# Kernel optimization log

Measured on AMD Instinct MI355X. Metric: run time of the kernel, lower is better.

## Reference

```python
import jax, jax.numpy as jnp
import numpy as np

B, S, H, L = 64, 512, 768, 3

def setup_inputs() -> dict:
    key = jax.random.key(0)
    ks = jax.random.split(key, 6)
    hidden = jax.random.normal(ks[0], (B, S, H), dtype=jnp.float32)
    attention_mask = jnp.ones((B, S), dtype=jnp.int32)
    labels = jax.random.randint(ks[1], (B, S), 0, L)
    W = jax.random.normal(ks[2], (H, L), dtype=jnp.float32) * 0.02
    b = jnp.zeros((L,), dtype=jnp.float32)
    start_transitions = jax.random.normal(ks[3], (L,), dtype=jnp.float32) * 0.1
    end_transitions = jax.random.normal(ks[4], (L,), dtype=jnp.float32) * 0.1
    transitions = jax.random.normal(ks[5], (L, L), dtype=jnp.float32) * 0.1
    return {"hidden": hidden, "W": W, "b": b,
            "start_transitions": start_transitions,
            "end_transitions": end_transitions,
            "transitions": transitions,
            "attention_mask": attention_mask, "labels": labels}

def _crf_nll(emissions, tags, mask, start_transitions, end_transitions, transitions):
    # emissions [B,S,L], tags [B,S] int, mask [B,S] float (contiguous, mask[:,0]=1)
    em_t = jnp.transpose(emissions, (1, 0, 2))   # [S,B,L]
    tags_t = tags.T                              # [S,B]
    mask_t = mask.T                              # [S,B]

    # --- gold-path score ---
    e0 = jnp.take_along_axis(em_t[0], tags_t[0][:, None], axis=1)[:, 0]
    score0 = start_transitions[tags_t[0]] + e0   # [B]

    def gold_step(carry, inp):
        score, prev_tags, last_tags = carry
        em, tg, m = inp
        e = jnp.take_along_axis(em, tg[:, None], axis=1)[:, 0]
        t = transitions[prev_tags, tg]
        score = score + (e + t) * m
        last_tags = jnp.where(m > 0, tg, last_tags)
        return (score, tg, last_tags), None

    (score, _, last_tags), _ = jax.lax.scan(
        gold_step, (score0, tags_t[0], tags_t[0]),
        (em_t[1:], tags_t[1:], mask_t[1:]))
    score = score + end_transitions[last_tags]   # [B]

    # --- log-partition via forward algorithm ---
    alpha0 = start_transitions[None, :] + em_t[0]  # [B,L]

    def fwd_step(alpha, inp):
        em, m = inp
        # [B,prev,next]: alpha + transition + next emission
        nxt = jax.nn.logsumexp(alpha[:, :, None] + transitions[None, :, :]
                               + em[:, None, :], axis=1)
        alpha = jnp.where(m[:, None] > 0, nxt, alpha)
        return alpha, None

    alpha, _ = jax.lax.scan(fwd_step, alpha0, (em_t[1:], mask_t[1:]))
    log_z = jax.nn.logsumexp(alpha + end_transitions[None, :], axis=1)  # [B]

    return -jnp.mean(score - log_z)  # reduction='mean', negated

def reference(hidden, W, b, start_transitions, end_transitions, transitions,
              attention_mask, labels):
    # classifier (dropout is identity in eval)
    emissions = hidden @ W + b                     # [B,S,L]
    crf_labels = jnp.where(labels < 0, 0, labels)  # masked_fill(labels<0, O)
    maskf = attention_mask.astype(emissions.dtype)
    loss = _crf_nll(emissions, crf_labels, maskf,
                    start_transitions, end_transitions, transitions)
    return loss
```

## Files before the change

kernel.cpp:

```cpp
#include <hip/hip_runtime.h>
#include <math.h>

#define HD 768
#define NL 3
#define BB 64
#define SS 512
#define NEG (-1e30f)

__device__ __forceinline__ float lse3(float x, float y, float z) {
    float m = fmaxf(fmaxf(x, y), z);
    return m + __logf(__expf(x - m) + __expf(y - m) + __expf(z - m));
}

__global__ __launch_bounds__(256) void emis_kernel(
    const float* __restrict__ hidden, const float* __restrict__ W,
    const float* __restrict__ bias, float* __restrict__ em) {
    int gid  = blockIdx.x * blockDim.x + threadIdx.x;
    int wave = gid >> 6;
    int lane = threadIdx.x & 63;
    int BS = BB * SS;
    if (wave >= BS) return;
    const float4* h4 = (const float4*)(hidden + (size_t)wave * HD);
    float a0 = 0.f, a1 = 0.f, a2 = 0.f;
#pragma unroll
    for (int i = 0; i < 3; ++i) {
        int k4 = lane + 64 * i;
        float4 v = h4[k4];
        int k = k4 * 4;
        a0 = fmaf(v.x, W[(k + 0) * 3 + 0], a0);
        a1 = fmaf(v.x, W[(k + 0) * 3 + 1], a1);
        a2 = fmaf(v.x, W[(k + 0) * 3 + 2], a2);
        a0 = fmaf(v.y, W[(k + 1) * 3 + 0], a0);
        a1 = fmaf(v.y, W[(k + 1) * 3 + 1], a1);
        a2 = fmaf(v.y, W[(k + 1) * 3 + 2], a2);
        a0 = fmaf(v.z, W[(k + 2) * 3 + 0], a0);
        a1 = fmaf(v.z, W[(k + 2) * 3 + 1], a1);
        a2 = fmaf(v.z, W[(k + 2) * 3 + 2], a2);
        a0 = fmaf(v.w, W[(k + 3) * 3 + 0], a0);
        a1 = fmaf(v.w, W[(k + 3) * 3 + 1], a1);
        a2 = fmaf(v.w, W[(k + 3) * 3 + 2], a2);
    }
#pragma unroll
    for (int off = 32; off; off >>= 1) {
        a0 += __shfl_down(a0, off);
        a1 += __shfl_down(a1, off);
        a2 += __shfl_down(a2, off);
    }
    if (lane == 0) {
        int b = wave >> 9;
        int s = wave & (SS - 1);
        float* o = em + ((size_t)b * SS + s) * NL;
        o[0] = a0 + bias[0];
        o[1] = a1 + bias[1];
        o[2] = a2 + bias[2];
    }
}

__global__ __launch_bounds__(64) void crf_scan_kernel(
    const float* __restrict__ em,
    const int* __restrict__ mask,
    const int* __restrict__ labels,
    const float* __restrict__ startT, const float* __restrict__ endT,
    const float* __restrict__ trans, float* __restrict__ part) {
    int b = blockIdx.x;
    int l = threadIdx.x;

    float T00 = trans[0], T01 = trans[1], T02 = trans[2];
    float T10 = trans[3], T11 = trans[4], T12 = trans[5];
    float T20 = trans[6], T21 = trans[7], T22 = trans[8];

    const float* emb = em + (size_t)b * SS * NL;
    const int*   tg  = labels + b * SS;
    const int*   mk  = mask + b * SS;
    int s0 = l * 8;

    const float4* ep = (const float4*)(emb + (size_t)s0 * NL);
    float4 E0 = ep[0], E1 = ep[1], E2 = ep[2];
    float4 E3 = ep[3], E4 = ep[4], E5 = ep[5];
    int4 ta  = ((const int4*)(tg + s0))[0];
    int4 tb4 = ((const int4*)(tg + s0))[1];
    int4 ma  = ((const int4*)(mk + s0))[0];
    int4 mb4 = ((const int4*)(mk + s0))[1];
    int pv = (l > 0) ? tg[s0 - 1] : 0;
    int prev = pv < 0 ? 0 : pv;

    float P00, P01, P02, P10, P11, P12, P20, P21, P22;
    float gold = 0.f;
    int last_s = -1, last_t = 0;

#define GOLD(kk, ee0, ee1, ee2, tt, mm, ACT)                                   \
    int t = (tt) < 0 ? 0 : (tt);                                               \
    bool act = (ACT) && ((mm) != 0);                                           \
    {                                                                          \
        float ev = (t == 0) ? (ee0) : ((t == 1) ? (ee1) : (ee2));              \
        float r0 = (t == 0) ? T00 : ((t == 1) ? T01 : T02);                    \
        float r1 = (t == 0) ? T10 : ((t == 1) ? T11 : T12);                    \
        float r2 = (t == 0) ? T20 : ((t == 1) ? T21 : T22);                    \
        float tpt = (prev == 0) ? r0 : ((prev == 1) ? r1 : r2);                \
        gold += act ? (ev + tpt) : 0.f;                                        \
        last_t = act ? t : last_t;                                             \
        last_s = act ? (s0 + (kk)) : last_s;                                   \
        prev = t;                                                              \
    }

#define STEP0(ee0, ee1, ee2, tt, mm) {                                         \
    GOLD(0, ee0, ee1, ee2, tt, mm, (s0 > 0))                                   \
    P00 = act ? (T00 + (ee0)) : 0.f;                                           \
    P01 = act ? (T01 + (ee1)) : NEG;                                           \
    P02 = act ? (T02 + (ee2)) : NEG;                                           \
    P10 = act ? (T10 + (ee0)) : NEG;                                           \
    P11 = act ? (T11 + (ee1)) : 0.f;                                           \
    P12 = act ? (T12 + (ee2)) : NEG;                                           \
    P20 = act ? (T20 + (ee0)) : NEG;                                           \
    P21 = act ? (T21 + (ee1)) : NEG;                                           \
    P22 = act ? (T22 + (ee2)) : 0.f;                                           \
}

#define STEPK(kk, ee0, ee1, ee2, tt, mm) {                                     \
    GOLD(kk, ee0, ee1, ee2, tt, mm, true)                                      \
    float n00 = lse3(P00 + T00, P01 + T10, P02 + T20) + (ee0);                 \
    float n01 = lse3(P00 + T01, P01 + T11, P02 + T21) + (ee1);                 \
    float n02 = lse3(P00 + T02, P01 + T12, P02 + T22) + (ee2);                 \
    float n10 = lse3(P10 + T00, P11 + T10, P12 + T20) + (ee0);                 \
    float n11 = lse3(P10 + T01, P11 + T11, P12 + T21) + (ee1);                 \
    float n12 = lse3(P10 + T02, P11 + T12, P12 + T22) + (ee2);                 \
    float n20 = lse3(P20 + T00, P21 + T10, P22 + T20) + (ee0);                 \
    float n21 = lse3(P20 + T01, P21 + T11, P22 + T21) + (ee1);                 \
    float n22 = lse3(P20 + T02, P21 + T12, P22 + T22) + (ee2);                 \
    P00 = act ? n00 : P00; P01 = act ? n01 : P01; P02 = act ? n02 : P02;       \
    P10 = act ? n10 : P10; P11 = act ? n11 : P11; P12 = act ? n12 : P12;       \
    P20 = act ? n20 : P20; P21 = act ? n21 : P21; P22 = act ? n22 : P22;       \
}

    STEP0(    E0.x, E0.y, E0.z, ta.x,  ma.x)
    STEPK(1,  E0.w, E1.x, E1.y, ta.y,  ma.y)
    STEPK(2,  E1.z, E1.w, E2.x, ta.z,  ma.z)
    STEPK(3,  E2.y, E2.z, E2.w, ta.w,  ma.w)
    STEPK(4,  E3.x, E3.y, E3.z, tb4.x, mb4.x)
    STEPK(5,  E3.w, E4.x, E4.y, tb4.y, mb4.y)
    STEPK(6,  E4.z, E4.w, E5.x, tb4.z, mb4.z)
    STEPK(7,  E5.y, E5.z, E5.w, tb4.w, mb4.w)

#pragma unroll
    for (int off = 1; off < 64; off <<= 1) {
        float B00 = __shfl_down(P00, off), B01 = __shfl_down(P01, off);
        float B02 = __shfl_down(P02, off), B10 = __shfl_down(P10, off);
        float B11 = __shfl_down(P11, off), B12 = __shfl_down(P12, off);
        float B20 = __shfl_down(P20, off), B21 = __shfl_down(P21, off);
        float B22 = __shfl_down(P22, off);
        float n00 = lse3(P00 + B00, P01 + B10, P02 + B20);
        float n01 = lse3(P00 + B01, P01 + B11, P02 + B21);
        float n02 = lse3(P00 + B02, P01 + B12, P02 + B22);
        float n10 = lse3(P10 + B00, P11 + B10, P12 + B20);
        float n11 = lse3(P10 + B01, P11 + B11, P12 + B21);
        float n12 = lse3(P10 + B02, P11 + B12, P12 + B22);
        float n20 = lse3(P20 + B00, P21 + B10, P22 + B20);
        float n21 = lse3(P20 + B01, P21 + B11, P22 + B21);
        float n22 = lse3(P20 + B02, P21 + B12, P22 + B22);
        P00 = n00; P01 = n01; P02 = n02;
        P10 = n10; P11 = n11; P12 = n12;
        P20 = n20; P21 = n21; P22 = n22;

        gold += __shfl_down(gold, off);
        int os = __shfl_down(last_s, off);
        int ot = __shfl_down(last_t, off);
        if (os > last_s) { last_s = os; last_t = ot; }
    }

    if (l == 0) {
        int t0 = ta.x < 0 ? 0 : ta.x;
        float st0 = startT[0], st1 = startT[1], st2 = startT[2];
        float en0 = endT[0],   en1 = endT[1],   en2 = endT[2];
        float e00 = E0.x, e01 = E0.y, e02 = E0.z;
        float a0 = st0 + e00, a1 = st1 + e01, a2 = st2 + e02;
        float f0 = lse3(a0 + P00, a1 + P10, a2 + P20);
        float f1 = lse3(a0 + P01, a1 + P11, a2 + P21);
        float f2 = lse3(a0 + P02, a1 + P12, a2 + P22);
        float logZ = lse3(f0 + en0, f1 + en1, f2 + en2);
        float sc0 = ((t0 == 0) ? st0 : ((t0 == 1) ? st1 : st2)) +
                    ((t0 == 0) ? e00 : ((t0 == 1) ? e01 : e02));
        if (last_s < 0) last_t = t0;
        float endv = (last_t == 0) ? en0 : ((last_t == 1) ? en1 : en2);
        float score = sc0 + gold + endv;
        part[b] = logZ - score;
    }
}

__global__ __launch_bounds__(64) void mean_kernel(
    const float* __restrict__ part, float* __restrict__ out) {
    float v = part[threadIdx.x];
#pragma unroll
    for (int off = 32; off; off >>= 1) v += __shfl_down(v, off);
    if (threadIdx.x == 0) out[0] = v * (1.0f / BB);
}

extern "C" void kernel_launch(void* const* d_in, const int* in_sizes, int n_in,
                              void* d_out, int out_size, void* d_ws, size_t ws_size,
                              hipStream_t stream) {
    const float* hidden = (const float*)d_in[0];
    const float* W      = (const float*)d_in[1];
    const float* bias   = (const float*)d_in[2];
    const float* startT = (const float*)d_in[3];
    const float* endT   = (const float*)d_in[4];
    const float* trans  = (const float*)d_in[5];
    const int*   mask   = (const int*)d_in[6];
    const int*   labels = (const int*)d_in[7];
    float* out = (float*)d_out;

    float* em   = (float*)d_ws;
    float* part = em + (size_t)BB * SS * NL;

    int BS = BB * SS;
    int blocks = BS / 4;
    emis_kernel<<<blocks, 256, 0, stream>>>(hidden, W, bias, em);
    crf_scan_kernel<<<BB, 64, 0, stream>>>(em, mask, labels, startT, endT,
                                           trans, part);
    mean_kernel<<<1, 64, 0, stream>>>(part, out);
}
```

Baseline: 31.89 us.

## Split CRF scan into four chunks per sequence with a combine kernel

```diff
diff --git a/kernel.cpp b/kernel.cpp
--- a/kernel.cpp
+++ b/kernel.cpp
@@ -56,14 +56,16 @@
     }
 }
 
-__global__ __launch_bounds__(64) void crf_scan_kernel(
+__global__ __launch_bounds__(64) void crf_part_kernel(
     const float* __restrict__ em,
     const int* __restrict__ mask,
     const int* __restrict__ labels,
-    const float* __restrict__ startT, const float* __restrict__ endT,
     const float* __restrict__ trans, float* __restrict__ part) {
-    int b = blockIdx.x;
+    int idx = blockIdx.x;
+    int b = idx & 63;
+    int c = idx >> 6;
     int l = threadIdx.x;
+    int s0 = c * 128 + l * 2;
 
     float T00 = trans[0], T01 = trans[1], T02 = trans[2];
     float T10 = trans[3], T11 = trans[4], T12 = trans[5];
@@ -72,25 +74,21 @@
     const float* emb = em + (size_t)b * SS * NL;
     const int*   tg  = labels + b * SS;
     const int*   mk  = mask + b * SS;
-    int s0 = l * 8;
-
-    const float4* ep = (const float4*)(emb + (size_t)s0 * NL);
-    float4 E0 = ep[0], E1 = ep[1], E2 = ep[2];
-    float4 E3 = ep[3], E4 = ep[4], E5 = ep[5];
-    int4 ta  = ((const int4*)(tg + s0))[0];
-    int4 tb4 = ((const int4*)(tg + s0))[1];
-    int4 ma  = ((const int4*)(mk + s0))[0];
-    int4 mb4 = ((const int4*)(mk + s0))[1];
-    int pv = (l > 0) ? tg[s0 - 1] : 0;
+
+    const float2* e2 = (const float2*)(emb + (size_t)s0 * NL);
+    float2 v01 = e2[0], v23 = e2[1], v45 = e2[2];
+    int2 tt = *(const int2*)(tg + s0);
+    int2 mm = *(const int2*)(mk + s0);
+    int pv = (s0 > 0) ? tg[s0 - 1] : 0;
     int prev = pv < 0 ? 0 : pv;
 
     float P00, P01, P02, P10, P11, P12, P20, P21, P22;
     float gold = 0.f;
     int last_s = -1, last_t = 0;
 
-#define GOLD(kk, ee0, ee1, ee2, tt, mm, ACT)                                   \
-    int t = (tt) < 0 ? 0 : (tt);                                               \
-    bool act = (ACT) && ((mm) != 0);                                           \
+#define GOLD(kk, ee0, ee1, ee2, tv, mv, ACT)                                   \
+    int t = (tv) < 0 ? 0 : (tv);                                               \
+    bool act = (ACT) && ((mv) != 0);                                           \
     {                                                                          \
         float ev = (t == 0) ? (ee0) : ((t == 1) ? (ee1) : (ee2));              \
         float r0 = (t == 0) ? T00 : ((t == 1) ? T01 : T02);                    \
@@ -103,8 +101,8 @@
         prev = t;                                                              \
     }
 
-#define STEP0(ee0, ee1, ee2, tt, mm) {                                         \
-    GOLD(0, ee0, ee1, ee2, tt, mm, (s0 > 0))                                   \
+#define STEP0(ee0, ee1, ee2, tv, mv) {                                         \
+    GOLD(0, ee0, ee1, ee2, tv, mv, (s0 > 0))                                   \
     P00 = act ? (T00 + (ee0)) : 0.f;                                           \
     P01 = act ? (T01 + (ee1)) : NEG;                                           \
     P02 = act ? (T02 + (ee2)) : NEG;                                           \
@@ -116,8 +114,8 @@
     P22 = act ? (T22 + (ee2)) : 0.f;                                           \
 }
 
-#define STEPK(kk, ee0, ee1, ee2, tt, mm) {                                     \
-    GOLD(kk, ee0, ee1, ee2, tt, mm, true)                                      \
+#define STEPK(kk, ee0, ee1, ee2, tv, mv) {                                     \
+    GOLD(kk, ee0, ee1, ee2, tv, mv, true)                                      \
     float n00 = lse3(P00 + T00, P01 + T10, P02 + T20) + (ee0);                 \
     float n01 = lse3(P00 + T01, P01 + T11, P02 + T21) + (ee1);                 \
     float n02 = lse3(P00 + T02, P01 + T12, P02 + T22) + (ee2);                 \
@@ -132,14 +130,8 @@
     P20 = act ? n20 : P20; P21 = act ? n21 : P21; P22 = act ? n22 : P22;       \
 }
 
-    STEP0(    E0.x, E0.y, E0.z, ta.x,  ma.x)
-    STEPK(1,  E0.w, E1.x, E1.y, ta.y,  ma.y)
-    STEPK(2,  E1.z, E1.w, E2.x, ta.z,  ma.z)
-    STEPK(3,  E2.y, E2.z, E2.w, ta.w,  ma.w)
-    STEPK(4,  E3.x, E3.y, E3.z, tb4.x, mb4.x)
-    STEPK(5,  E3.w, E4.x, E4.y, tb4.y, mb4.y)
-    STEPK(6,  E4.z, E4.w, E5.x, tb4.z, mb4.z)
-    STEPK(7,  E5.y, E5.z, E5.w, tb4.w, mb4.w)
+    STEP0(    v01.x, v01.y, v23.x, tt.x, mm.x)
+    STEPK(1,  v23.y, v45.x, v45.y, tt.y, mm.y)
 
 #pragma unroll
     for (int off = 1; off < 64; off <<= 1) {
@@ -168,30 +160,84 @@
     }
 
     if (l == 0) {
-        int t0 = ta.x < 0 ? 0 : ta.x;
-        float st0 = startT[0], st1 = startT[1], st2 = startT[2];
-        float en0 = endT[0],   en1 = endT[1],   en2 = endT[2];
-        float e00 = E0.x, e01 = E0.y, e02 = E0.z;
-        float a0 = st0 + e00, a1 = st1 + e01, a2 = st2 + e02;
-        float f0 = lse3(a0 + P00, a1 + P10, a2 + P20);
-        float f1 = lse3(a0 + P01, a1 + P11, a2 + P21);
-        float f2 = lse3(a0 + P02, a1 + P12, a2 + P22);
-        float logZ = lse3(f0 + en0, f1 + en1, f2 + en2);
-        float sc0 = ((t0 == 0) ? st0 : ((t0 == 1) ? st1 : st2)) +
-                    ((t0 == 0) ? e00 : ((t0 == 1) ? e01 : e02));
-        if (last_s < 0) last_t = t0;
-        float endv = (last_t == 0) ? en0 : ((last_t == 1) ? en1 : en2);
-        float score = sc0 + gold + endv;
-        part[b] = logZ - score;
-    }
-}
-
-__global__ __launch_bounds__(64) void mean_kernel(
-    const float* __restrict__ part, float* __restrict__ out) {
-    float v = part[threadIdx.x];
-#pragma unroll
-    for (int off = 32; off; off >>= 1) v += __shfl_down(v, off);
-    if (threadIdx.x == 0) out[0] = v * (1.0f / BB);
+        float4* dst = (float4*)part + ((size_t)c * BB + b) * 3;
+        float4 q0 = {P00, P01, P02, P10};
+        float4 q1 = {P11, P12, P20, P21};
+        float4 q2 = {P22, gold, __int_as_float(last_s), __int_as_float(last_t)};
+        dst[0] = q0; dst[1] = q1; dst[2] = q2;
+    }
+}
+
+struct M3 { float a00,a01,a02,a10,a11,a12,a20,a21,a22; };
+
+__device__ __forceinline__ M3 otimes(const M3& P, const M3& B) {
+    M3 N;
+    N.a00 = lse3(P.a00 + B.a00, P.a01 + B.a10, P.a02 + B.a20);
+    N.a01 = lse3(P.a00 + B.a01, P.a01 + B.a11, P.a02 + B.a21);
+    N.a02 = lse3(P.a00 + B.a02, P.a01 + B.a12, P.a02 + B.a22);
+    N.a10 = lse3(P.a10 + B.a00, P.a11 + B.a10, P.a12 + B.a20);
+    N.a11 = lse3(P.a10 + B.a01, P.a11 + B.a11, P.a12 + B.a21);
+    N.a12 = lse3(P.a10 + B.a02, P.a11 + B.a12, P.a12 + B.a22);
+    N.a20 = lse3(P.a20 + B.a00, P.a21 + B.a10, P.a22 + B.a20);
+    N.a21 = lse3(P.a20 + B.a01, P.a21 + B.a11, P.a22 + B.a21);
+    N.a22 = lse3(P.a20 + B.a02, P.a21 + B.a12, P.a22 + B.a22);
+    return N;
+}
+
+__global__ __launch_bounds__(64) void crf_combine_kernel(
+    const float* __restrict__ part, const float* __restrict__ em,
+    const int* __restrict__ labels,
+    const float* __restrict__ startT, const float* __restrict__ endT,
+    float* __restrict__ out) {
+    int b = threadIdx.x;
+    const float4* pp = (const float4*)part;
+
+    float4 a0 = pp[(0 * BB + b) * 3 + 0], a1 = pp[(0 * BB + b) * 3 + 1],
+           a2 = pp[(0 * BB + b) * 3 + 2];
+    float4 b0 = pp[(1 * BB + b) * 3 + 0], b1 = pp[(1 * BB + b) * 3 + 1],
+           b2 = pp[(1 * BB + b) * 3 + 2];
+    float4 c0 = pp[(2 * BB + b) * 3 + 0], c1 = pp[(2 * BB + b) * 3 + 1],
+           c2 = pp[(2 * BB + b) * 3 + 2];
+    float4 d0 = pp[(3 * BB + b) * 3 + 0], d1 = pp[(3 * BB + b) * 3 + 1],
+           d2 = pp[(3 * BB + b) * 3 + 2];
+
+    M3 R  = {a0.x, a0.y, a0.z, a0.w, a1.x, a1.y, a1.z, a1.w, a2.x};
+    M3 M1 = {b0.x, b0.y, b0.z, b0.w, b1.x, b1.y, b1.z, b1.w, b2.x};
+    M3 M2 = {c0.x, c0.y, c0.z, c0.w, c1.x, c1.y, c1.z, c1.w, c2.x};
+    M3 M3v = {d0.x, d0.y, d0.z, d0.w, d1.x, d1.y, d1.z, d1.w, d2.x};
+    R = otimes(R, M1);
+    R = otimes(R, M2);
+    R = otimes(R, M3v);
+
+    float gold = a2.y + b2.y + c2.y + d2.y;
+    int last_s = __float_as_int(a2.z), last_t = __float_as_int(a2.w);
+    int s1 = __float_as_int(b2.z), t1 = __float_as_int(b2.w);
+    int s2 = __float_as_int(c2.z), t2 = __float_as_int(c2.w);
+    int s3 = __float_as_int(d2.z), t3 = __float_as_int(d2.w);
+    if (s1 > last_s) { last_s = s1; last_t = t1; }
+    if (s2 > last_s) { last_s = s2; last_t = t2; }
+    if (s3 > last_s) { last_s = s3; last_t = t3; }
+
+    const float* emb = em + (size_t)b * SS * NL;
+    float e00 = emb[0], e01 = emb[1], e02 = emb[2];
+    int t0 = labels[b * SS]; t0 = t0 < 0 ? 0 : t0;
+    float st0 = startT[0], st1 = startT[1], st2 = startT[2];
+    float en0 = endT[0],   en1 = endT[1],   en2 = endT[2];
+
+    float al0 = st0 + e00, al1 = st1 + e01, al2 = st2 + e02;
+    float f0 = lse3(al0 + R.a00, al1 + R.a10, al2 + R.a20);
+    float f1 = lse3(al0 + R.a01, al1 + R.a11, al2 + R.a21);
+    float f2 = lse3(al0 + R.a02, al1 + R.a12, al2 + R.a22);
+    float logZ = lse3(f0 + en0, f1 + en1, f2 + en2);
+    float sc0 = ((t0 == 0) ? st0 : ((t0 == 1) ? st1 : st2)) +
+                ((t0 == 0) ? e00 : ((t0 == 1) ? e01 : e02));
+    if (last_s < 0) last_t = t0;
+    float endv = (last_t == 0) ? en0 : ((last_t == 1) ? en1 : en2);
+    float contrib = logZ - (sc0 + gold + endv);
+
+#pragma unroll
+    for (int off = 32; off; off >>= 1) contrib += __shfl_down(contrib, off);
+    if (b == 0) out[0] = contrib * (1.0f / BB);
 }
 
 extern "C" void kernel_launch(void* const* d_in, const int* in_sizes, int n_in,
@@ -213,7 +259,6 @@
     int BS = BB * SS;
     int blocks = BS / 4;
     emis_kernel<<<blocks, 256, 0, stream>>>(hidden, W, bias, em);
-    crf_scan_kernel<<<BB, 64, 0, stream>>>(em, mask, labels, startT, endT,
-                                           trans, part);
-    mean_kernel<<<1, 64, 0, stream>>>(part, out);
-}
+    crf_part_kernel<<<4 * BB, 64, 0, stream>>>(em, mask, labels, trans, part);
+    crf_combine_kernel<<<1, 64, 0, stream>>>(part, em, labels, startT, endT, out);
+}
```

After: 29.97 us (median of 2 runs). -6.0%, faster.
